# Optimization experiments

Hardware: AMD Instinct MI355X
Metric: run time of the kernel (lower is better)

Reference implementation:

```python
import jax, jax.numpy as jnp
import numpy as np

EPS = 1e-5

def _rmsnorm(x, w):
    return x * jax.lax.rsqrt(jnp.mean(x * x, axis=-1, keepdims=True) + EPS) * w


def setup_inputs() -> dict:
    key = jax.random.key(0)
    ks = jax.random.split(key, 12)
    b, l, d = 2, 4096, 1024
    expand, d_state, d_conv, headdim = 2, 128, 4, 64
    d_inner = d * expand            # 2048
    nheads = d_inner // headdim     # 32
    conv_dim = d_inner + 2 * d_state            # 2304 (x, B, C; ngroups=1)
    d_in_proj = 2 * d_inner + 2 * d_state + nheads  # z, xBC, dt
    s = 0.02
    return {
        "x": jax.random.normal(ks[0], (b, l, d), jnp.float32),
        "norm_w": jnp.ones((d,), jnp.float32),
        "in_proj_W": jax.random.normal(ks[1], (d, d_in_proj), jnp.float32) * s,
        "conv_W": jax.random.normal(ks[2], (d_conv, conv_dim), jnp.float32) * s,
        "conv_b": jnp.zeros((conv_dim,), jnp.float32),
        "dt_bias": jax.random.normal(ks[3], (nheads,), jnp.float32) * 0.5,
        "A_log": jnp.log(jnp.arange(1, nheads + 1, dtype=jnp.float32)),
        "D": jnp.ones((nheads,), jnp.float32),
        "gnorm_w": jnp.ones((d_inner,), jnp.float32),
        "zero_W": jax.random.normal(ks[4], (d, d_inner), jnp.float32) * s,
        "one_W": jax.random.normal(ks[5], (d, d_inner), jnp.float32) * s,
        "fusion_W": jax.random.normal(ks[6], (3 * d_inner, d), jnp.float32) * s,
    }


def _mamba2(xn, in_proj_W, conv_W, conv_b, dt_bias, A_log, D, gnorm_w):
    b, l, _ = xn.shape
    nheads = dt_bias.shape[0]
    conv_dim = conv_W.shape[1]
    d_state = (conv_W.shape[1] - gnorm_w.shape[0]) // 2
    d_inner = gnorm_w.shape[0]
    headdim = d_inner // nheads

    zxbcdt = xn @ in_proj_W                         # (b,l, 2*d_inner+2*n+h)
    z = zxbcdt[..., :d_inner]
    xBC = zxbcdt[..., d_inner:d_inner + conv_dim]
    dt = zxbcdt[..., -nheads:]

    # causal depthwise conv over seq, kernel size d_conv
    d_conv = conv_W.shape[0]
    pad = jnp.pad(xBC, ((0, 0), (d_conv - 1, 0), (0, 0)))
    conv = conv_b
    for k in range(d_conv):
        conv = conv + pad[:, k:k + l, :] * conv_W[k]
    xBC = jax.nn.silu(conv)

    xs = xBC[..., :d_inner].reshape(b, l, nheads, headdim)   # (b,l,h,p)
    Bm = xBC[..., d_inner:d_inner + d_state]                 # (b,l,n)
    Cm = xBC[..., d_inner + d_state:]                        # (b,l,n)

    dt = jax.nn.softplus(dt + dt_bias)                       # (b,l,h)
    A = -jnp.exp(A_log)                                      # (h,)
    dA = jnp.exp(dt * A)                                     # (b,l,h)

    def step(state, inp):
        dA_t, dt_t, B_t, C_t, x_t = inp   # (b,h),(b,h),(b,n),(b,n),(b,h,p)
        state = state * dA_t[:, :, None, None] + \
            (dt_t[:, :, None] * x_t)[..., None] * B_t[:, None, None, :]
        y_t = jnp.einsum('bhpn,bn->bhp', state, C_t)
        return state, y_t

    state0 = jnp.zeros((b, nheads, headdim, d_state), xn.dtype)
    inps = (dA.transpose(1, 0, 2), dt.transpose(1, 0, 2),
            Bm.transpose(1, 0, 2), Cm.transpose(1, 0, 2),
            xs.transpose(1, 0, 2, 3))
    _, ys = jax.lax.scan(step, state0, inps)                 # (l,b,h,p)
    y = ys.transpose(1, 0, 2, 3) + D[None, None, :, None] * xs
    y = y.reshape(b, l, d_inner)
    return _rmsnorm(y * jax.nn.silu(z), gnorm_w)             # (b,l,d_inner)


def reference(x, norm_w, in_proj_W, conv_W, conv_b, dt_bias, A_log, D,
              gnorm_w, zero_W, one_W, fusion_W):
    residual = x
    xn = _rmsnorm(x, norm_w)
    mamba_out = _mamba2(xn, in_proj_W, conv_W, conv_b, dt_bias, A_log, D, gnorm_w)
    y_zero = xn @ zero_W
    y_one = jnp.cumsum(xn @ one_W, axis=1)
    fused = jnp.concatenate([mamba_out, y_zero, y_one], axis=-1)
    return residual + fused @ fusion_W
```

## Files before the change

### kernel.cpp

```cpp
#include <hip/hip_runtime.h>
#include <hip/hip_bf16.h>
#include <stdint.h>

#define BATCH   2
#define SEQL    4096
#define DMODEL  1024
#define DIN     2048
#define NH      32
#define HDIM    64
#define DSTATE  128
#define CONVD   2304
#define DPROJ   4384
#define NTOT    8192
#define NBIG    6528
#define NREAL   6432
#define NPAD    6656
#define CHT     128
#define NCH     32
#define SP      136

typedef __attribute__((ext_vector_type(8))) short short8;
typedef __attribute__((ext_vector_type(4))) float f32x4;

__device__ __forceinline__ unsigned short f2bf(float f) {
    unsigned int u = __builtin_bit_cast(unsigned int, f);
    return (unsigned short)((u + 0x7FFFu + ((u >> 16) & 1u)) >> 16);
}
__device__ __forceinline__ float bf2f(unsigned short u) {
    unsigned int v = ((unsigned int)u) << 16;
    return __builtin_bit_cast(float, v);
}

__device__ __forceinline__ void gload16(const void* g, void* l) {
    __builtin_amdgcn_global_load_lds(
        (const __attribute__((address_space(1))) unsigned int*)g,
        (__attribute__((address_space(3))) unsigned int*)l,
        16, 0, 0);
}

__global__ void transpose_cast_kernel(const float* __restrict__ in,
                                      unsigned short* __restrict__ out,
                                      int R, int C) {
    __shared__ float tile[32][33];
    int c0 = blockIdx.x * 32, r0 = blockIdx.y * 32;
    int tx = threadIdx.x, ty = threadIdx.y;
    #pragma unroll
    for (int i = ty; i < 32; i += 8)
        tile[i][tx] = in[(size_t)(r0 + i) * C + c0 + tx];
    __syncthreads();
    #pragma unroll
    for (int i = ty; i < 32; i += 8)
        out[(size_t)(c0 + i) * R + r0 + tx] = f2bf(tile[tx][i]);
}

__global__ void cast_bf16_kernel(const float* __restrict__ in,
                                 unsigned short* __restrict__ out, int n4) {
    int i = (blockIdx.x * 256 + threadIdx.x) * 4;
    if (i < n4) {
        float4 v = *(const float4*)(in + i);
        ushort4 o;
        o.x = f2bf(v.x); o.y = f2bf(v.y); o.z = f2bf(v.z); o.w = f2bf(v.w);
        *(ushort4*)(out + i) = o;
    }
}

__global__ void zero_pad_kernel(unsigned short* __restrict__ p, int n) {
    int i = blockIdx.x * 256 + threadIdx.x;
    if (i < n) p[i] = 0;
}

__global__ __launch_bounds__(256) void rmsnorm_cast_kernel(
    const float* __restrict__ x, const float* __restrict__ w,
    unsigned short* __restrict__ xn) {
    int tok = blockIdx.x, tid = threadIdx.x;
    float4 v = ((const float4*)(x + (size_t)tok * DMODEL))[tid];
    float ss = v.x*v.x + v.y*v.y + v.z*v.z + v.w*v.w;
    #pragma unroll
    for (int off = 32; off > 0; off >>= 1) ss += __shfl_xor(ss, off, 64);
    __shared__ float sred[4];
    if ((tid & 63) == 0) sred[tid >> 6] = ss;
    __syncthreads();
    float tot = sred[0] + sred[1] + sred[2] + sred[3];
    float r = rsqrtf(tot * (1.0f / DMODEL) + 1e-5f);
    float4 wv = ((const float4*)w)[tid];
    ushort4 o;
    o.x = f2bf(v.x * r * wv.x); o.y = f2bf(v.y * r * wv.y);
    o.z = f2bf(v.z * r * wv.z); o.w = f2bf(v.w * r * wv.w);
    ((ushort4*)(xn + (size_t)tok * DMODEL))[tid] = o;
}

__global__ __launch_bounds__(512, 2) void gemm256_kernel(
    const unsigned short* __restrict__ A, int lda,
    const unsigned short* __restrict__ B, int ldb,
    unsigned short* __restrict__ Cout, int ldc, int K, int Nreal) {
    __shared__ __align__(16) unsigned short lds[8][8192];
    const int tid = threadIdx.x;
    const int nkt = K >> 6;
    const int ghalves = nkt << 2;

    int nwg = gridDim.x * gridDim.y;
    int orig = blockIdx.y * gridDim.x + blockIdx.x;
    int q8 = nwg >> 3;
    int wgid = (orig & 7) * q8 + (orig >> 3);
    int W = gridDim.x * 4;
    int band = wgid / W, rem = wgid % W;
    int bm = band * 4 + (rem & 3), bn = rem >> 2;

    const int wave = tid >> 6, lane = tid & 63;
    const int wm = wave >> 2, wn = wave & 3;
    const int quad = lane >> 4, l15 = lane & 15;
    const int cpos = (((l15 & 1) << 2) + quad + (l15 >> 1)) & 7;
    const int aoff = wm * 4096 + (l15 >> 1) * 64 + cpos * 8;
    const int boff = wn * 2048 + (l15 >> 1) * 64 + cpos * 8;

    const int srow = tid >> 3;
    const int dch  = tid & 7;
    const int ech  = (dch - srow) & 7;
    const int g_r0 = 2 * srow + (ech >> 2);
    const int g_c0 = (ech & 3) * 8;
    const unsigned short* A0 = A + (size_t)(bm * 256 + g_r0) * lda + g_c0;
    const unsigned short* A1 = A0 + (size_t)128 * lda;
    const unsigned short* B0 = B + (size_t)(bn * 256 + g_r0) * ldb + g_c0;
    const unsigned short* B1 = B0 + (size_t)128 * ldb;

    auto stage = [&](int g) {
        int tg = g >> 2, idx = g & 3;
        int k0 = tg * 64 + ((idx >> 1) << 5);
        unsigned short* d = &lds[g & 7][tid * 8];
        if (idx & 1) { gload16(B0 + k0, d); gload16(B1 + k0, d + 4096); }
        else         { gload16(A0 + k0, d); gload16(A1 + k0, d + 4096); }
    };

    f32x4 acc[8][4] = {};
    stage(0); stage(1); stage(2); stage(3);
    asm volatile("s_waitcnt vmcnt(4)");
    stage(4); stage(5); stage(6);
    asm volatile("s_waitcnt vmcnt(6)");
    __builtin_amdgcn_s_barrier();

    short8 a[8], b[2];
    for (int t = 0; t < nkt; ++t) {
        #pragma unroll
        for (int ph = 0; ph < 4; ++ph) {
            const int kk = ph >> 1, nq = ph & 1;
            const unsigned short* As = lds[(4 * t + 2 * kk) & 7];
            const unsigned short* Bs = lds[(4 * t + 2 * kk + 1) & 7];
            if (nq == 0) {
                #pragma unroll
                for (int m = 0; m < 8; ++m)
                    a[m] = *(const short8*)&As[aoff + m * 512];
            }
            b[0] = *(const short8*)&Bs[boff + (nq * 2) * 512];
            b[1] = *(const short8*)&Bs[boff + (nq * 2 + 1) * 512];
            int g = 4 * t + 7 + ph;
            if (g < ghalves) stage(g);
            __builtin_amdgcn_s_barrier();
            asm volatile("s_waitcnt lgkmcnt(0)");
            __builtin_amdgcn_s_setprio(1);
            #pragma unroll
            for (int m = 0; m < 8; ++m) {
                acc[m][nq * 2]     = __builtin_amdgcn_mfma_f32_16x16x32_bf16(
                    a[m], b[0], acc[m][nq * 2], 0, 0, 0);
                acc[m][nq * 2 + 1] = __builtin_amdgcn_mfma_f32_16x16x32_bf16(
                    a[m], b[1], acc[m][nq * 2 + 1], 0, 0, 0);
            }
            __builtin_amdgcn_s_setprio(0);
            if (ph == 3) {
                if (t == nkt - 2) asm volatile("s_waitcnt vmcnt(0)");
                else              asm volatile("s_waitcnt vmcnt(6)");
            }
            __builtin_amdgcn_s_barrier();
        }
    }

    const int rbase = bm * 256 + wm * 128 + quad * 4;
    const int cb0 = bn * 256 + wn * 64 + l15;
    #pragma unroll
    for (int m = 0; m < 8; ++m) {
        #pragma unroll
        for (int n = 0; n < 4; ++n) {
            int cb = cb0 + n * 16;
            if (cb < Nreal) {
                unsigned short* cp = Cout + (size_t)(rbase + m * 16) * ldc + cb;
                #pragma unroll
                for (int r = 0; r < 4; ++r)
                    cp[(size_t)r * ldc] = f2bf(acc[m][n][r]);
            }
        }
    }
}

template<int MODE>
__global__ __launch_bounds__(256) void gemm_bt_kernel(
    const unsigned short* __restrict__ A, int lda,
    const unsigned short* __restrict__ B, int ldb,
    void* __restrict__ Cout, int ldc, int K,
    const float* __restrict__ addX, const unsigned short* __restrict__ Zbuf) {
    __shared__ __align__(16) unsigned short sA[128 * 64];
    __shared__ __align__(16) unsigned short sB[128 * 64];
    int tid = threadIdx.x;
    int bid = blockIdx.y * gridDim.x + blockIdx.x;
    int W = gridDim.x * 8;
    int band = bid / W, rem = bid % W;
    int bn = rem >> 3, bm = band * 8 + (rem & 7);
    int wave = tid >> 6, lane = tid & 63;
    int wm = wave >> 1, wn = wave & 1;
    f32x4 acc[4][4] = {};
    const unsigned short* Ab = A + (size_t)(bm * 128) * lda;
    const unsigned short* Bb = B + (size_t)(bn * 128) * ldb;
    int sRow = tid >> 3;
    int srcoff = (((tid & 7) - (tid >> 3)) & 7) * 8;
    int quad = lane >> 4, l15 = lane & 15;
    for (int k0 = 0; k0 < K; k0 += 64) {
        __syncthreads();
        #pragma unroll
        for (int it = 0; it < 4; ++it) {
            int row = sRow + it * 32;
            gload16(&Ab[(size_t)row * lda + k0 + srcoff], &sA[it * 2048 + tid * 8]);
            gload16(&Bb[(size_t)row * ldb + k0 + srcoff], &sB[it * 2048 + tid * 8]);
        }
        __syncthreads();
        #pragma unroll
        for (int kk = 0; kk < 64; kk += 32) {
            short8 a[4], b[4];
            #pragma unroll
            for (int i = 0; i < 4; ++i) {
                int mr = wm * 64 + i * 16 + l15;
                a[i] = *(const short8*)&sA[mr * 64 + (((kk >> 3) + quad + mr) & 7) * 8];
                int nr = wn * 64 + i * 16 + l15;
                b[i] = *(const short8*)&sB[nr * 64 + (((kk >> 3) + quad + nr) & 7) * 8];
            }
            #pragma unroll
            for (int i = 0; i < 4; ++i)
                #pragma unroll
                for (int j = 0; j < 4; ++j)
                    acc[i][j] = __builtin_amdgcn_mfma_f32_16x16x32_bf16(
                        a[i], b[j], acc[i][j], 0, 0, 0);
        }
    }
    int rbase = bm * 128 + wm * 64 + quad * 4;
    int cbase = bn * 128 + wn * 64 + l15;
    #pragma unroll
    for (int i = 0; i < 4; ++i) {
        #pragma unroll
        for (int r = 0; r < 4; ++r) {
            int gr = rbase + i * 16 + r;
            if constexpr (MODE == 1) {
                unsigned short* crow = (unsigned short*)Cout + (size_t)gr * ldc + cbase;
                #pragma unroll
                for (int j = 0; j < 4; ++j) crow[j * 16] = f2bf(acc[i][j][r]);
            } else {
                float* crow = (float*)Cout + (size_t)gr * ldc + cbase;
                const float* xr = addX + (size_t)gr * DMODEL + cbase;
                const unsigned short* zrow = Zbuf + (size_t)gr * NBIG;
                const float* qrow = (const float*)zrow;
                #pragma unroll
                for (int j = 0; j < 4; ++j)
                    crow[j * 16] = acc[i][j][r] + xr[j * 16]
                                 + bf2f(zrow[4384 + cbase + j * 16])
                                 + qrow[cbase + j * 16];
            }
        }
    }
}

__global__ __launch_bounds__(256) void gemm64_kernel(
    const unsigned short* __restrict__ A, int lda,
    const unsigned short* __restrict__ B, int ldb,
    unsigned short* __restrict__ Cout, int ldc, int K) {
    __shared__ __align__(16) unsigned short sA[64 * 64];
    __shared__ __align__(16) unsigned short sB[64 * 64];
    int tid = threadIdx.x;
    int bn = blockIdx.x, bm = blockIdx.y;
    int wave = tid >> 6, lane = tid & 63;
    int wm = wave >> 1, wn = wave & 1;
    f32x4 acc[2][2] = {};
    const unsigned short* Ab = A + (size_t)(bm * 64) * lda;
    const unsigned short* Bb = B + (size_t)(bn * 64) * ldb;
    int sRow = tid >> 3;
    int srcoff = (((tid & 7) - (tid >> 3)) & 7) * 8;
    int quad = lane >> 4, l15 = lane & 15;
    for (int k0 = 0; k0 < K; k0 += 64) {
        __syncthreads();
        #pragma unroll
        for (int it = 0; it < 2; ++it) {
            int row = sRow + it * 32;
            gload16(&Ab[(size_t)row * lda + k0 + srcoff], &sA[it * 2048 + tid * 8]);
            gload16(&Bb[(size_t)row * ldb + k0 + srcoff], &sB[it * 2048 + tid * 8]);
        }
        __syncthreads();
        #pragma unroll
        for (int kk = 0; kk < 64; kk += 32) {
            short8 a[2], b[2];
            #pragma unroll
            for (int i = 0; i < 2; ++i) {
                int mr = wm * 32 + i * 16 + l15;
                a[i] = *(const short8*)&sA[mr * 64 + (((kk >> 3) + quad + mr) & 7) * 8];
                int nr = wn * 32 + i * 16 + l15;
                b[i] = *(const short8*)&sB[nr * 64 + (((kk >> 3) + quad + nr) & 7) * 8];
            }
            #pragma unroll
            for (int i = 0; i < 2; ++i)
                #pragma unroll
                for (int j = 0; j < 2; ++j)
                    acc[i][j] = __builtin_amdgcn_mfma_f32_16x16x32_bf16(
                        a[i], b[j], acc[i][j], 0, 0, 0);
        }
    }
    int rbase = bm * 64 + wm * 32 + quad * 4;
    int cbase = bn * 64 + wn * 32 + l15;
    #pragma unroll
    for (int i = 0; i < 2; ++i)
        #pragma unroll
        for (int r = 0; r < 4; ++r) {
            int gr = rbase + i * 16 + r;
            unsigned short* crow = Cout + (size_t)gr * ldc + cbase;
            #pragma unroll
            for (int j = 0; j < 2; ++j) crow[j * 16] = f2bf(acc[i][j][r]);
        }
}

__global__ __launch_bounds__(256) void conv_silu_kernel(
    const unsigned short* __restrict__ Z, const float* __restrict__ convW,
    const float* __restrict__ convB, unsigned short* __restrict__ xbc) {
    int tok = blockIdx.x;
    int bi = tok >> 12, t = tok & 4095;
    for (int c = threadIdx.x; c < CONVD; c += 256) {
        float acc = convB[c];
        #pragma unroll
        for (int k = 0; k < 4; ++k) {
            int tt = t - 3 + k;
            if (tt >= 0)
                acc += bf2f(Z[(size_t)(bi * SEQL + tt) * NBIG + 2048 + c]) * convW[k * CONVD + c];
        }
        xbc[(size_t)tok * CONVD + c] = f2bf(acc / (1.0f + expf(-acc)));
    }
}

__global__ __launch_bounds__(256, 2) void chunk_intra_kernel(
    const unsigned short* __restrict__ xbc, const unsigned short* __restrict__ Z,
    const float* __restrict__ dt_bias, const float* __restrict__ A_log,
    unsigned short* __restrict__ TS, float* __restrict__ abuf,
    unsigned short* __restrict__ ym) {
    __shared__ __align__(16) unsigned short Xt[64 * SP];
    __shared__ __align__(16) unsigned short Xw[64 * SP];
    __shared__ __align__(16) unsigned short BtM[128 * SP];
    __shared__ float dt_lds[128], dtA_lds[128], cum_lds[128], w_lds[128];
    int tid = threadIdx.x;
    int kch = blockIdx.x, bh = blockIdx.y;
    int h = bh & 31, bi = bh >> 5;
    int tok0 = bi * SEQL + kch * CHT;
    const unsigned short* xb = xbc + (size_t)tok0 * CONVD;
    if (tid < 128) {
        float v = bf2f(Z[(size_t)(tok0 + tid) * NBIG + 4352 + h]) + dt_bias[h];
        float sp = (v > 20.f) ? v : log1pf(expf(v));
        dt_lds[tid] = sp;
        dtA_lds[tid] = -sp * expf(A_log[h]);
    }
    for (int seg = tid; seg < 128 * 16; seg += 256) {
        int s = seg & 127, nb = seg >> 7;
        short8 v = *(const short8*)&xb[(size_t)s * CONVD + 2048 + nb * 8];
        #pragma unroll
        for (int j = 0; j < 8; ++j) BtM[(nb * 8 + j) * SP + s] = (unsigned short)v[j];
    }
    for (int seg = tid; seg < 128 * 8; seg += 256) {
        int s = seg & 127, pb = seg >> 7;
        short8 v = *(const short8*)&xb[(size_t)s * CONVD + h * 64 + pb * 8];
        #pragma unroll
        for (int j = 0; j < 8; ++j) Xt[(pb * 8 + j) * SP + s] = (unsigned short)v[j];
    }
    __syncthreads();
    if (tid < 128) {
        int lw = tid & 63;
        float v = dtA_lds[tid];
        #pragma unroll
        for (int off = 1; off < 64; off <<= 1) {
            float o = __shfl_up(v, off, 64);
            if (lw >= off) v += o;
        }
        cum_lds[tid] = v;
    }
    __syncthreads();
    if (tid >= 64 && tid < 128) cum_lds[tid] += cum_lds[63];
    __syncthreads();
    if (tid < 128) {
        float cT = cum_lds[127];
        w_lds[tid] = __expf(cT - cum_lds[tid]) * dt_lds[tid];
        abuf[(size_t)(bh * NCH + kch) * 128 + tid] = __expf(cum_lds[tid]);
    }
    __syncthreads();
    for (int seg = tid; seg < 64 * 16; seg += 256) {
        int pp = seg >> 4, sb = seg & 15;
        short8 v = *(const short8*)&Xt[pp * SP + sb * 8];
        short8 o;
        #pragma unroll
        for (int j = 0; j < 8; ++j)
            o[j] = (short)f2bf(bf2f((unsigned short)v[j]) * w_lds[sb * 8 + j]);
        *(short8*)&Xw[pp * SP + sb * 8] = o;
    }
    __syncthreads();
    int lane = tid & 63, wv = tid >> 6;
    int quad = lane >> 4, l15 = lane & 15;
    {
        f32x4 acc[8] = {};
        for (int kk = 0; kk < 128; kk += 32) {
            short8 a = *(const short8*)&Xw[(16 * wv + l15) * SP + kk + quad * 8];
            #pragma unroll
            for (int jn = 0; jn < 8; ++jn) {
                short8 b = *(const short8*)&BtM[(16 * jn + l15) * SP + kk + quad * 8];
                acc[jn] = __builtin_amdgcn_mfma_f32_16x16x32_bf16(a, b, acc[jn], 0, 0, 0);
            }
        }
        size_t tsbase = (size_t)(bh * NCH + kch) * 8192;
        #pragma unroll
        for (int jn = 0; jn < 8; ++jn)
            #pragma unroll
            for (int r = 0; r < 4; ++r) {
                int pp = 16 * wv + quad * 4 + r, n = 16 * jn + l15;
                TS[tsbase + pp * 128 + n] = f2bf(acc[jn][r]);
            }
    }
    __syncthreads();
    {
        f32x4 g[2][8] = {};
        for (int kk = 0; kk < 128; kk += 32) {
            int co = 2176 + kk + quad * 8;
            short8 a0 = *(const short8*)&xb[(size_t)(32 * wv + l15) * CONVD + co];
            short8 a1 = *(const short8*)&xb[(size_t)(32 * wv + 16 + l15) * CONVD + co];
            int bo = 2048 + kk + quad * 8;
            #pragma unroll
            for (int js = 0; js < 8; ++js) {
                short8 b = *(const short8*)&xb[(size_t)(16 * js + l15) * CONVD + bo];
                g[0][js] = __builtin_amdgcn_mfma_f32_16x16x32_bf16(a0, b, g[0][js], 0, 0, 0);
                g[1][js] = __builtin_amdgcn_mfma_f32_16x16x32_bf16(a1, b, g[1][js], 0, 0, 0);
            }
        }
        #pragma unroll
        for (int it = 0; it < 2; ++it)
            #pragma unroll
            for (int js = 0; js < 8; ++js) {
                int s = 16 * js + l15;
                float cs = cum_lds[s], ds = dt_lds[s];
                #pragma unroll
                for (int r = 0; r < 4; ++r) {
                    int t = 32 * wv + 16 * it + quad * 4 + r;
                    float f = (s <= t) ? __expf(cum_lds[t] - cs) * ds : 0.f;
                    BtM[t * SP + s] = f2bf(g[it][js][r] * f);
                }
            }
    }
    __syncthreads();
    {
        f32x4 y[2][4] = {};
        for (int kk = 0; kk < 128; kk += 32) {
            short8 a0 = *(const short8*)&BtM[(32 * wv + l15) * SP + kk + quad * 8];
            short8 a1 = *(const short8*)&BtM[(32 * wv + 16 + l15) * SP + kk + quad * 8];
            #pragma unroll
            for (int jp = 0; jp < 4; ++jp) {
                short8 b = *(const short8*)&Xt[(16 * jp + l15) * SP + kk + quad * 8];
                y[0][jp] = __builtin_amdgcn_mfma_f32_16x16x32_bf16(a0, b, y[0][jp], 0, 0, 0);
                y[1][jp] = __builtin_amdgcn_mfma_f32_16x16x32_bf16(a1, b, y[1][jp], 0, 0, 0);
            }
        }
        #pragma unroll
        for (int it = 0; it < 2; ++it)
            #pragma unroll
            for (int jp = 0; jp < 4; ++jp)
                #pragma unroll
                for (int r = 0; r < 4; ++r) {
                    int t = 32 * wv + 16 * it + quad * 4 + r;
                    int pp = 16 * jp + l15;
                    ym[(size_t)(tok0 + t) * DIN + h * 64 + pp] = f2bf(y[it][jp][r]);
                }
    }
}

__global__ __launch_bounds__(128) void state_recur_kernel(
    unsigned short* __restrict__ TS, const float* __restrict__ abuf) {
    int bh = blockIdx.x >> 6, p = blockIdx.x & 63, n = threadIdx.x;
    float s = 0.f;
    for (int k = 0; k < NCH; ++k) {
        size_t base = ((size_t)(bh * NCH + k) * 64 + p) * 128 + n;
        float aT = abuf[(size_t)(bh * NCH + k) * 128 + 127];
        float tv = bf2f(TS[base]);
        TS[base] = f2bf(s);
        s = fmaf(aT, s, tv);
    }
}

__global__ __launch_bounds__(256) void chunk_inter_kernel(
    const unsigned short* __restrict__ xbc, const unsigned short* __restrict__ TS,
    const float* __restrict__ abuf, const float* __restrict__ Dp,
    unsigned short* ym) {
    __shared__ float a_ld[128];
    int tid = threadIdx.x;
    int kch = blockIdx.x, bh = blockIdx.y;
    int h = bh & 31, bi = bh >> 5;
    int tok0 = bi * SEQL + kch * CHT;
    if (tid < 128) a_ld[tid] = abuf[(size_t)(bh * NCH + kch) * 128 + tid];
    __syncthreads();
    int lane = tid & 63, wv = tid >> 6;
    int quad = lane >> 4, l15 = lane & 15;
    const unsigned short* xb = xbc + (size_t)tok0 * CONVD;
    size_t tsbase = (size_t)(bh * NCH + kch) * 8192;
    int t0 = 32 * wv + l15, t1 = t0 + 16;
    float at0 = a_ld[t0], at1 = a_ld[t1];
    f32x4 y[2][4] = {};
    for (int kk = 0; kk < 128; kk += 32) {
        int co = 2176 + kk + quad * 8;
        short8 c0 = *(const short8*)&xb[(size_t)t0 * CONVD + co];
        short8 c1 = *(const short8*)&xb[(size_t)t1 * CONVD + co];
        short8 a0, a1;
        #pragma unroll
        for (int j = 0; j < 8; ++j) {
            a0[j] = (short)f2bf(bf2f((unsigned short)c0[j]) * at0);
            a1[j] = (short)f2bf(bf2f((unsigned short)c1[j]) * at1);
        }
        #pragma unroll
        for (int jp = 0; jp < 4; ++jp) {
            short8 b = *(const short8*)&TS[tsbase + (size_t)(16 * jp + l15) * 128 + kk + quad * 8];
            y[0][jp] = __builtin_amdgcn_mfma_f32_16x16x32_bf16(a0, b, y[0][jp], 0, 0, 0);
            y[1][jp] = __builtin_amdgcn_mfma_f32_16x16x32_bf16(a1, b, y[1][jp], 0, 0, 0);
        }
    }
    float Dh = Dp[h];
    #pragma unroll
    for (int it = 0; it < 2; ++it)
        #pragma unroll
        for (int jp = 0; jp < 4; ++jp)
            #pragma unroll
            for (int r = 0; r < 4; ++r) {
                int t = 32 * wv + 16 * it + quad * 4 + r;
                int pp = 16 * jp + l15;
                size_t yi = (size_t)(tok0 + t) * DIN + h * 64 + pp;
                float xv = bf2f(xb[(size_t)t * CONVD + h * 64 + pp]);
                float yv = y[it][jp][r] + bf2f(ym[yi]) + Dh * xv;
                ym[yi] = f2bf(yv);
            }
}

__global__ __launch_bounds__(256) void gated_norm_kernel(
    const unsigned short* __restrict__ y,
    const unsigned short* __restrict__ Z,
    const float* __restrict__ gw, unsigned short* mamba) {
    int tok = blockIdx.x, tid = threadIdx.x;
    float vals[8];
    float ss = 0;
    #pragma unroll
    for (int i = 0; i < 8; ++i) {
        int c = tid + i * 256;
        float yv = bf2f(y[(size_t)tok * DIN + c]);
        float zv = bf2f(Z[(size_t)tok * NBIG + c]);
        float g = yv * (zv / (1.0f + expf(-zv)));
        vals[i] = g;
        ss += g * g;
    }
    #pragma unroll
    for (int off = 32; off > 0; off >>= 1) ss += __shfl_xor(ss, off, 64);
    __shared__ float sred[4];
    if ((tid & 63) == 0) sred[tid >> 6] = ss;
    __syncthreads();
    float tot = sred[0] + sred[1] + sred[2] + sred[3];
    float r = rsqrtf(tot * (1.0f / DIN) + 1e-5f);
    #pragma unroll
    for (int i = 0; i < 8; ++i) {
        int c = tid + i * 256;
        mamba[(size_t)tok * DIN + c] = f2bf(vals[i] * r * gw[c]);
    }
}

__global__ void cumsum_pass1_kernel(const unsigned short* __restrict__ Z,
                                    float* __restrict__ S) {
    int cg = blockIdx.x & 3, ch = (blockIdx.x >> 2) & 31, bi = blockIdx.x >> 7;
    int c = cg * 256 + threadIdx.x;
    size_t base = (size_t)(bi * SEQL + ch * 128) * NBIG;
    float s = 0;
    for (int t = 0; t < 128; ++t)
        s += bf2f(Z[base + (size_t)t * NBIG + 5408 + c]);
    S[(bi * 32 + ch) * 1024 + c] = s;
}

__global__ void cumsum_pass2_kernel(unsigned short* __restrict__ Z,
                                    const float* __restrict__ S) {
    int cg = blockIdx.x & 3, ch = (blockIdx.x >> 2) & 31, bi = blockIdx.x >> 7;
    int c = cg * 256 + threadIdx.x;
    float run = 0;
    for (int k = 0; k < ch; ++k) run += S[(bi * 32 + k) * 1024 + c];
    size_t base = (size_t)(bi * SEQL + ch * 128) * NBIG;
    for (int t = 0; t < 128; ++t) {
        size_t row = base + (size_t)t * NBIG;
        run += bf2f(Z[row + 5408 + c]);
        ((float*)(Z + row))[c] = run;
    }
}

extern "C" void kernel_launch(void* const* d_in, const int* in_sizes, int n_in,
                              void* d_out, int out_size, void* d_ws, size_t ws_size,
                              hipStream_t stream) {
    (void)in_sizes; (void)n_in; (void)out_size; (void)ws_size;
    const float* x        = (const float*)d_in[0];
    const float* norm_w   = (const float*)d_in[1];
    const float* in_projW = (const float*)d_in[2];
    const float* conv_W   = (const float*)d_in[3];
    const float* conv_b   = (const float*)d_in[4];
    const float* dt_bias  = (const float*)d_in[5];
    const float* A_log    = (const float*)d_in[6];
    const float* Dp       = (const float*)d_in[7];
    const float* gnorm_w  = (const float*)d_in[8];
    const float* zero_W   = (const float*)d_in[9];
    const float* one_W    = (const float*)d_in[10];
    const float* fusion_W = (const float*)d_in[11];
    float* out = (float*)d_out;

    char* p = (char*)d_ws;
    auto alloc = [&](size_t bytes) { char* r = p; p += (bytes + 255) & ~(size_t)255; return r; };
    unsigned short* Wf_t  = (unsigned short*)alloc((size_t)DMODEL * 6144 * 2);
    char* pool0 = p;
    unsigned short* xn_bf = (unsigned short*)alloc((size_t)NTOT * DMODEL * 2);
    unsigned short* zWb   = (unsigned short*)alloc((size_t)DMODEL * DIN * 2);
    unsigned short* oWb   = (unsigned short*)alloc((size_t)DMODEL * DIN * 2);
    unsigned short* Bt    = (unsigned short*)alloc((size_t)NPAD * DMODEL * 2);
    unsigned short* xbc   = (unsigned short*)pool0;
    float* abuf = (float*)alloc((size_t)64 * NCH * 128 * 4);
    float* Sb   = (float*)alloc((size_t)2 * 32 * 1024 * 4);
    unsigned short* ym  = (unsigned short*)alloc((size_t)NTOT * DIN * 2);
    unsigned short* Zbf = (unsigned short*)alloc((size_t)NTOT * NBIG * 2);
    unsigned short* TS = (unsigned short*)d_out;

    transpose_cast_kernel<<<dim3(DPROJ / 32, DMODEL / 32), dim3(32, 8), 0, stream>>>(
        in_projW, Bt, DMODEL, DPROJ);
    transpose_cast_kernel<<<dim3(DMODEL / 32, 6144 / 32), dim3(32, 8), 0, stream>>>(
        fusion_W, Wf_t, 6144, DMODEL);
    cast_bf16_kernel<<<2048, 256, 0, stream>>>(zero_W, zWb, DMODEL * DIN);
    cast_bf16_kernel<<<2048, 256, 0, stream>>>(one_W, oWb, DMODEL * DIN);
    zero_pad_kernel<<<(NPAD - NREAL) * DMODEL / 256, 256, 0, stream>>>(
        Bt + (size_t)NREAL * DMODEL, (NPAD - NREAL) * DMODEL);

    rmsnorm_cast_kernel<<<NTOT, 256, 0, stream>>>(x, norm_w, xn_bf);

    gemm64_kernel<<<dim3(16, 16), 256, 0, stream>>>(
        Wf_t + 2048, 6144, zWb, DIN, Bt + (size_t)4384 * DMODEL, DMODEL, DIN);
    gemm64_kernel<<<dim3(16, 16), 256, 0, stream>>>(
        Wf_t + 4096, 6144, oWb, DIN, Bt + (size_t)5408 * DMODEL, DMODEL, DIN);

    gemm256_kernel<<<dim3(NPAD / 256, NTOT / 256), 512, 0, stream>>>(
        xn_bf, DMODEL, Bt, DMODEL, Zbf, NBIG, DMODEL, NBIG);

    conv_silu_kernel<<<NTOT, 256, 0, stream>>>(Zbf, conv_W, conv_b, xbc);

    chunk_intra_kernel<<<dim3(NCH, 64), 256, 0, stream>>>(
        xbc, Zbf, dt_bias, A_log, TS, abuf, ym);
    state_recur_kernel<<<64 * 64, 128, 0, stream>>>(TS, abuf);
    chunk_inter_kernel<<<dim3(NCH, 64), 256, 0, stream>>>(
        xbc, TS, abuf, Dp, ym);

    gated_norm_kernel<<<NTOT, 256, 0, stream>>>(ym, Zbf, gnorm_w, ym);

    cumsum_pass1_kernel<<<256, 256, 0, stream>>>(Zbf, Sb);
    cumsum_pass2_kernel<<<256, 256, 0, stream>>>(Zbf, Sb);

    gemm_bt_kernel<2><<<dim3(DMODEL / 128, NTOT / 128), 256, 0, stream>>>(
        ym, DIN, Wf_t, 6144, out, DMODEL, DIN, x, Zbf);
}
```

Before: 642.0 us.

## Restructure GEMM main loop into double-buffered register ping-pong with LDS/MFMA overlap

Rewrites the bf16 GEMM inner loop so A/B fragments are double-buffered in registers (a[2][4], b[2][4]) and the next quarter-tile's LDS reads are issued before the current 4x4 MFMA block runs. Partial lgkmcnt waits replace full waits so LDS latency hides behind MFMA work. The loop is unrolled by two tiles via a macro so the 8-slot LDS ring indices become compile-time constants. This raises register pressure, and it assumes nkt is even and that the retuned vmcnt counts are correct.

```diff
diff --git a/kernel.cpp b/kernel.cpp
--- a/kernel.cpp
+++ b/kernel.cpp
@@ -131,47 +131,99 @@
         else         { gload16(A0 + k0, d); gload16(A1 + k0, d + 4096); }
     };
 
+    short8 a[2][4], b[2][4];
     f32x4 acc[8][4] = {};
-    stage(0); stage(1); stage(2); stage(3);
-    asm volatile("s_waitcnt vmcnt(4)");
-    stage(4); stage(5); stage(6);
-    asm volatile("s_waitcnt vmcnt(6)");
+
+    stage(0); stage(1); stage(2); stage(3); stage(4); stage(5); stage(6);
+    asm volatile("s_waitcnt vmcnt(10)" ::: "memory");
     __builtin_amdgcn_s_barrier();
-
-    short8 a[8], b[2];
-    for (int t = 0; t < nkt; ++t) {
-        #pragma unroll
-        for (int ph = 0; ph < 4; ++ph) {
-            const int kk = ph >> 1, nq = ph & 1;
-            const unsigned short* As = lds[(4 * t + 2 * kk) & 7];
-            const unsigned short* Bs = lds[(4 * t + 2 * kk + 1) & 7];
-            if (nq == 0) {
-                #pragma unroll
-                for (int m = 0; m < 8; ++m)
-                    a[m] = *(const short8*)&As[aoff + m * 512];
-            }
-            b[0] = *(const short8*)&Bs[boff + (nq * 2) * 512];
-            b[1] = *(const short8*)&Bs[boff + (nq * 2 + 1) * 512];
-            int g = 4 * t + 7 + ph;
-            if (g < ghalves) stage(g);
-            __builtin_amdgcn_s_barrier();
-            asm volatile("s_waitcnt lgkmcnt(0)");
-            __builtin_amdgcn_s_setprio(1);
-            #pragma unroll
-            for (int m = 0; m < 8; ++m) {
-                acc[m][nq * 2]     = __builtin_amdgcn_mfma_f32_16x16x32_bf16(
-                    a[m], b[0], acc[m][nq * 2], 0, 0, 0);
-                acc[m][nq * 2 + 1] = __builtin_amdgcn_mfma_f32_16x16x32_bf16(
-                    a[m], b[1], acc[m][nq * 2 + 1], 0, 0, 0);
-            }
-            __builtin_amdgcn_s_setprio(0);
-            if (ph == 3) {
-                if (t == nkt - 2) asm volatile("s_waitcnt vmcnt(0)");
-                else              asm volatile("s_waitcnt vmcnt(6)");
-            }
-            __builtin_amdgcn_s_barrier();
-        }
-    }
+    {
+        const unsigned short* As = lds[0];
+        const unsigned short* Bs = lds[1];
+        #pragma unroll
+        for (int i = 0; i < 4; ++i) a[0][i] = *(const short8*)&As[aoff + i * 512];
+        #pragma unroll
+        for (int j = 0; j < 4; ++j) b[0][j] = *(const short8*)&Bs[boff + j * 512];
+    }
+
+#define TILE_BODY(SB, t)                                                      \
+    {                                                                         \
+        const unsigned short* S0 = lds[(SB + 0) & 7];                         \
+        const unsigned short* S2 = lds[(SB + 2) & 7];                         \
+        const unsigned short* S3 = lds[(SB + 3) & 7];                         \
+        const unsigned short* S4 = lds[(SB + 4) & 7];                         \
+        const unsigned short* S5 = lds[(SB + 5) & 7];                         \
+        const int gbase = 4 * (t);                                            \
+                      \
+        _Pragma("unroll") for (int i = 0; i < 4; ++i)                         \
+            a[1][i] = *(const short8*)&S0[aoff + (4 + i) * 512];              \
+        asm volatile("s_waitcnt lgkmcnt(4)" ::: "memory");                    \
+        __builtin_amdgcn_s_barrier();                                         \
+        if (gbase + 7 < ghalves) stage(gbase + 7);                            \
+        __builtin_amdgcn_s_setprio(1);                                        \
+        _Pragma("unroll") for (int i = 0; i < 4; ++i)                         \
+            _Pragma("unroll") for (int j = 0; j < 4; ++j)                     \
+                acc[i][j] = __builtin_amdgcn_mfma_f32_16x16x32_bf16(          \
+                    a[0][i], b[0][j], acc[i][j], 0, 0, 0);                    \
+        __builtin_amdgcn_s_setprio(0);                                        \
+        if ((t) == nkt - 1) { asm volatile("s_waitcnt vmcnt(0)" ::: "memory"); } \
+        else                { asm volatile("s_waitcnt vmcnt(8)" ::: "memory"); } \
+        __builtin_amdgcn_s_barrier();                                         \
+               \
+        _Pragma("unroll") for (int i = 0; i < 4; ++i)                         \
+            a[0][i] = *(const short8*)&S2[aoff + i * 512];                    \
+        _Pragma("unroll") for (int j = 0; j < 4; ++j)                         \
+            b[1][j] = *(const short8*)&S3[boff + j * 512];                    \
+        asm volatile("s_waitcnt lgkmcnt(8)" ::: "memory");                    \
+        __builtin_amdgcn_s_barrier();                                         \
+        if (gbase + 8 < ghalves) stage(gbase + 8);                            \
+        __builtin_amdgcn_s_setprio(1);                                        \
+        _Pragma("unroll") for (int i = 0; i < 4; ++i)                         \
+            _Pragma("unroll") for (int j = 0; j < 4; ++j)                     \
+                acc[4 + i][j] = __builtin_amdgcn_mfma_f32_16x16x32_bf16(      \
+                    a[1][i], b[0][j], acc[4 + i][j], 0, 0, 0);                \
+        __builtin_amdgcn_s_setprio(0);                                        \
+        __builtin_amdgcn_s_barrier();                                         \
+                           \
+        _Pragma("unroll") for (int i = 0; i < 4; ++i)                         \
+            a[1][i] = *(const short8*)&S2[aoff + (4 + i) * 512];              \
+        asm volatile("s_waitcnt lgkmcnt(4)" ::: "memory");                    \
+        __builtin_amdgcn_s_barrier();                                         \
+        if (gbase + 9 < ghalves) stage(gbase + 9);                            \
+        __builtin_amdgcn_s_setprio(1);                                        \
+        _Pragma("unroll") for (int i = 0; i < 4; ++i)                         \
+            _Pragma("unroll") for (int j = 0; j < 4; ++j)                     \
+                acc[i][j] = __builtin_amdgcn_mfma_f32_16x16x32_bf16(          \
+                    a[0][i], b[1][j], acc[i][j], 0, 0, 0);                    \
+        __builtin_amdgcn_s_setprio(0);                                        \
+        if ((t) == nkt - 2)     { asm volatile("s_waitcnt vmcnt(4)" ::: "memory"); } \
+        else if ((t) < nkt - 2) { asm volatile("s_waitcnt vmcnt(8)" ::: "memory"); } \
+        __builtin_amdgcn_s_barrier();                                         \
+          \
+        if ((t) + 1 < nkt) {                                                  \
+            _Pragma("unroll") for (int i = 0; i < 4; ++i)                     \
+                a[0][i] = *(const short8*)&S4[aoff + i * 512];                \
+            _Pragma("unroll") for (int j = 0; j < 4; ++j)                     \
+                b[0][j] = *(const short8*)&S5[boff + j * 512];                \
+        }                                                                     \
+        asm volatile("s_waitcnt lgkmcnt(8)" ::: "memory");                    \
+        __builtin_amdgcn_s_barrier();                                         \
+        if (gbase + 10 < ghalves) stage(gbase + 10);                          \
+        __builtin_amdgcn_s_setprio(1);                                        \
+        _Pragma("unroll") for (int i = 0; i < 4; ++i)                         \
+            _Pragma("unroll") for (int j = 0; j < 4; ++j)                     \
+                acc[4 + i][j] = __builtin_amdgcn_mfma_f32_16x16x32_bf16(      \
+                    a[1][i], b[1][j], acc[4 + i][j], 0, 0, 0);                \
+        __builtin_amdgcn_s_setprio(0);                                        \
+        __builtin_amdgcn_s_barrier();                                         \
+    }
+
+    #pragma unroll 1
+    for (int t = 0; t < nkt; t += 2) {
+        TILE_BODY(0, t);
+        TILE_BODY(4, t + 1);
+    }
+#undef TILE_BODY
 
     const int rbase = bm * 256 + wm * 128 + quad * 4;
     const int cb0 = bn * 256 + wn * 64 + l15;
```

Result: slower. 771.5 us (+20.2%).
